# Kernel tuning notes

Hardware: AMD Instinct MI355X
Metric: run time of the kernel (lower is better)

## Reference

```python
import jax, jax.numpy as jnp
import numpy as np

TEMPERATURE = 0.1
LARGE_NUM = 1e9


def _l2_normalize(x, eps=1e-12):
    # tf.math.l2_normalize: x * rsqrt(max(sum(x^2), eps))
    sq = jnp.sum(x * x, axis=-1, keepdims=True)
    return x * jax.lax.rsqrt(jnp.maximum(sq, eps))


def setup_inputs() -> dict:
    key = jax.random.key(0)
    k1, k2 = jax.random.split(key)
    B, D = 4096, 128
    z1 = jax.random.normal(k1, (B, D), dtype=jnp.float32)
    z2 = jax.random.normal(k2, (B, D), dtype=jnp.float32)
    return {"z1": z1, "z2": z2}


def reference(z1, z2):
    B = z1.shape[0]
    a = _l2_normalize(z1)  # [B, D]
    b = _l2_normalize(z2)  # [B, D]
    mask = jnp.eye(B, dtype=a.dtype)
    inv_t = 1.0 / TEMPERATURE
    logits_aa = jnp.matmul(a, a.T) * inv_t - mask * LARGE_NUM  # [B, B]
    logits_bb = jnp.matmul(b, b.T) * inv_t - mask * LARGE_NUM  # [B, B]
    logits_ab = jnp.matmul(a, b.T) * inv_t                      # [B, B]
    logits_ba = jnp.matmul(b, a.T) * inv_t                      # [B, B]
    part1 = jax.nn.softmax(jnp.concatenate([logits_ab, logits_aa], axis=1), axis=-1)
    part2 = jax.nn.softmax(jnp.concatenate([logits_ba, logits_bb], axis=1), axis=-1)
    return jnp.concatenate([part1, part2], axis=1)  # [B, 4B]
```

## Files before the change

### kernel.cpp

```cpp
#include <hip/hip_runtime.h>
#include <hip/hip_fp16.h>
#include <cstdint>
#include <cstddef>

#define NB   4096
#define ND   128
#define OUTW 16384

#define K2   14.4269504088896341f

typedef _Float16 f16;
typedef __attribute__((ext_vector_type(2))) _Float16 f16x2;
typedef __attribute__((ext_vector_type(8))) _Float16 f16x8;
typedef __attribute__((ext_vector_type(4))) float   f32x4;

__global__ __launch_bounds__(256) void nrm_kernel(const float* __restrict__ z1,
                                                  const float* __restrict__ z2,
                                                  f16* __restrict__ ab,
                                                  float* __restrict__ rowsum) {
  if (threadIdx.x < 4) rowsum[blockIdx.x * 4 + threadIdx.x] = 0.0f;
  int row  = blockIdx.x * 4 + (threadIdx.x >> 6);
  int lane = threadIdx.x & 63;
  const float* src = (row < NB) ? (z1 + (size_t)row * ND)
                                : (z2 + (size_t)(row - NB) * ND);
  float2 v = ((const float2*)src)[lane];
  float ss = v.x * v.x + v.y * v.y;
#pragma unroll
  for (int off = 32; off; off >>= 1) ss += __shfl_xor(ss, off);
  float r = rsqrtf(fmaxf(ss, 1e-12f));
  f16x2 h;
  h.x = (f16)(v.x * r);
  h.y = (f16)(v.y * r);
  ((f16x2*)(ab + (size_t)row * ND))[lane] = h;
}

template <bool WRITE>
__global__ __launch_bounds__(256) void pass_kernel(const f16* __restrict__ ab,
                                                   float* __restrict__ rowsum,
                                                   float* __restrict__ out) {
  __shared__ f16 As[128 * ND];
  __shared__ f16 Bs[128 * ND];
  __shared__ float cs[128];

  const int t    = threadIdx.x;
  const int wave = t >> 6;
  const int lane = t & 63;
  const int rt   = blockIdx.y;
  const int ct   = blockIdx.x;
  const int type = rt >> 5;
  const int r0   = (rt & 31) * 128;
  const int c0l  = ct * 128;
  const int h2   = (c0l >= NB) ? 1 : 0;
  const int c0   = c0l & (NB - 1);
  const bool diag = h2 && (c0 == r0);
  const f16* Q = ab + (size_t)type * NB * ND;
  const f16* K = ab + (size_t)(h2 ^ type ^ 1) * NB * ND;

  {
    int sub = t >> 4;
    int oct = t & 15;
#pragma unroll
    for (int i = 0; i < 8; ++i) {
      int rowl = i * 16 + sub;
      int goct = oct ^ (rowl & 15);
      const f16* ga = Q + (size_t)(r0 + rowl) * ND + goct * 8;
      const f16* gb = K + (size_t)(c0 + rowl) * ND + goct * 8;
      __builtin_amdgcn_global_load_lds(
          (const __attribute__((address_space(1))) void*)ga,
          (__attribute__((address_space(3))) void*)(As + rowl * ND + oct * 8),
          16, 0, 0);
      __builtin_amdgcn_global_load_lds(
          (const __attribute__((address_space(1))) void*)gb,
          (__attribute__((address_space(3))) void*)(Bs + rowl * ND + oct * 8),
          16, 0, 0);
    }
  }
  if (WRITE) {
    if (t < 128) {
      float s = rowsum[rt * 128 + t];
      cs[t] = -__log2f(s) - K2;
    }
  }
  __syncthreads();

  const int wr   = wave >> 1;
  const int wc   = wave & 1;
  const int quad = lane >> 4;
  const int l16  = lane & 15;

  f32x4 acc[4][4] = {};
#pragma unroll
  for (int ks = 0; ks < 4; ++ks) {
    f16x8 af[4], bf[4];
    int oct = ks * 4 + quad;
    int sw  = (oct ^ l16) * 8;
#pragma unroll
    for (int mi = 0; mi < 4; ++mi)
      af[mi] = *(const f16x8*)(As + (wr * 64 + mi * 16 + l16) * ND + sw);
#pragma unroll
    for (int ni = 0; ni < 4; ++ni)
      bf[ni] = *(const f16x8*)(Bs + (wc * 64 + ni * 16 + l16) * ND + sw);
#pragma unroll
    for (int mi = 0; mi < 4; ++mi)
#pragma unroll
      for (int ni = 0; ni < 4; ++ni)
        acc[mi][ni] = __builtin_amdgcn_mfma_f32_16x16x32_f16(af[mi], bf[ni],
                                                             acc[mi][ni], 0, 0, 0);
  }

  if (WRITE) {
    float4 cf[4];
#pragma unroll
    for (int mi = 0; mi < 4; ++mi)
      cf[mi] = *(const float4*)&cs[wr * 64 + mi * 16 + quad * 4];
#pragma unroll
    for (int mi = 0; mi < 4; ++mi) {
#pragma unroll
      for (int ni = 0; ni < 4; ++ni) {
        int col_l = wc * 64 + ni * 16 + l16;
        int cg    = c0l + col_l;
        int rbase = wr * 64 + mi * 16 + quad * 4;
        const float* cp = &cf[mi].x;
#pragma unroll
        for (int r = 0; r < 4; ++r) {
          int row_l = rbase + r;
          int rg    = r0 + row_l;
          float e = __builtin_amdgcn_exp2f(fmaf(acc[mi][ni][r], K2, cp[r]));
          if (diag) { if (col_l == row_l) e = 0.0f; }
          out[(size_t)rg * OUTW + (size_t)type * 8192 + cg] = e;
        }
      }
    }
  } else {
#pragma unroll
    for (int mi = 0; mi < 4; ++mi) {
      float ps[4] = {0.f, 0.f, 0.f, 0.f};
#pragma unroll
      for (int ni = 0; ni < 4; ++ni) {
        int col_l = wc * 64 + ni * 16 + l16;
        int rbase = wr * 64 + mi * 16 + quad * 4;
#pragma unroll
        for (int r = 0; r < 4; ++r) {
          float e = __builtin_amdgcn_exp2f(fmaf(acc[mi][ni][r], K2, -K2));
          if (diag) { if (col_l == rbase + r) e = 0.0f; }
          ps[r] += e;
        }
      }
#pragma unroll
      for (int r = 0; r < 4; ++r) {
        float v = ps[r];
#pragma unroll
        for (int off = 1; off < 16; off <<= 1) v += __shfl_xor(v, off);
        if (l16 == 0) {
          int row_l = wr * 64 + mi * 16 + quad * 4 + r;
          atomicAdd(&rowsum[rt * 128 + row_l], v);
        }
      }
    }
  }
}

extern "C" void kernel_launch(void* const* d_in, const int* in_sizes, int n_in,
                              void* d_out, int out_size, void* d_ws, size_t ws_size,
                              hipStream_t stream) {
  const float* z1 = (const float*)d_in[0];
  const float* z2 = (const float*)d_in[1];
  float* out = (float*)d_out;

  f16* ab = (f16*)d_ws;
  float* rowsum = (float*)((char*)d_ws + (size_t)8192 * ND * sizeof(f16));

  nrm_kernel<<<2048, 256, 0, stream>>>(z1, z2, ab, rowsum);
  dim3 grid(64, 64);
  pass_kernel<false><<<grid, 256, 0, stream>>>(ab, rowsum, out);
  pass_kernel<true><<<grid, 256, 0, stream>>>(ab, rowsum, out);
}
```

Before: 356.7 us.

## Keep Q fragments in registers and stream double-buffered K tiles per block

Each block now owns a 128-row strip and loops over 8 column tiles of 64, instead of handling one 128x128 tile per block. The Q operand is loaded once into registers and reused across every column tile, while the K tiles are double-buffered in LDS through async global-to-LDS loads. Row partial sums are kept in registers across the whole strip, so each block issues far fewer atomics. The intent is to cut redundant Q loads, atomic traffic and block launch overhead, at the cost of fewer blocks (1024), higher register pressure and a serialized loop per block.

New measurement: 305.5 us. 14.4% less time.

```diff
diff --git a/kernel.cpp b/kernel.cpp
--- a/kernel.cpp
+++ b/kernel.cpp
@@ -6,6 +6,8 @@
 #define NB   4096
 #define ND   128
 #define OUTW 16384
+#define CG   16
+#define IT   (8192 / CG / 64)
 
 #define K2   14.4269504088896341f
 
@@ -35,120 +37,138 @@
 }
 
 template <bool WRITE>
-__global__ __launch_bounds__(256) void pass_kernel(const f16* __restrict__ ab,
-                                                   float* __restrict__ rowsum,
-                                                   float* __restrict__ out) {
-  __shared__ f16 As[128 * ND];
-  __shared__ f16 Bs[128 * ND];
+__global__ __launch_bounds__(256, 2) void pass_kernel(const f16* __restrict__ ab,
+                                                      float* __restrict__ rowsum,
+                                                      float* __restrict__ out) {
+  __shared__ f16 Bs[2][64 * ND];
   __shared__ float cs[128];
 
   const int t    = threadIdx.x;
   const int wave = t >> 6;
   const int lane = t & 63;
-  const int rt   = blockIdx.y;
-  const int ct   = blockIdx.x;
-  const int type = rt >> 5;
-  const int r0   = (rt & 31) * 128;
-  const int c0l  = ct * 128;
-  const int h2   = (c0l >= NB) ? 1 : 0;
-  const int c0   = c0l & (NB - 1);
-  const bool diag = h2 && (c0 == r0);
-  const f16* Q = ab + (size_t)type * NB * ND;
-  const f16* K = ab + (size_t)(h2 ^ type ^ 1) * NB * ND;
-
-  {
-    int sub = t >> 4;
-    int oct = t & 15;
-#pragma unroll
-    for (int i = 0; i < 8; ++i) {
-      int rowl = i * 16 + sub;
-      int goct = oct ^ (rowl & 15);
-      const f16* ga = Q + (size_t)(r0 + rowl) * ND + goct * 8;
-      const f16* gb = K + (size_t)(c0 + rowl) * ND + goct * 8;
-      __builtin_amdgcn_global_load_lds(
-          (const __attribute__((address_space(1))) void*)ga,
-          (__attribute__((address_space(3))) void*)(As + rowl * ND + oct * 8),
-          16, 0, 0);
-      __builtin_amdgcn_global_load_lds(
-          (const __attribute__((address_space(1))) void*)gb,
-          (__attribute__((address_space(3))) void*)(Bs + rowl * ND + oct * 8),
-          16, 0, 0);
-    }
-  }
-  if (WRITE) {
-    if (t < 128) {
-      float s = rowsum[rt * 128 + t];
-      cs[t] = -__log2f(s) - K2;
-    }
-  }
-  __syncthreads();
-
   const int wr   = wave >> 1;
   const int wc   = wave & 1;
   const int quad = lane >> 4;
   const int l16  = lane & 15;
 
-  f32x4 acc[4][4] = {};
-#pragma unroll
-  for (int ks = 0; ks < 4; ++ks) {
-    f16x8 af[4], bf[4];
-    int oct = ks * 4 + quad;
-    int sw  = (oct ^ l16) * 8;
-#pragma unroll
-    for (int mi = 0; mi < 4; ++mi)
-      af[mi] = *(const f16x8*)(As + (wr * 64 + mi * 16 + l16) * ND + sw);
-#pragma unroll
-    for (int ni = 0; ni < 4; ++ni)
-      bf[ni] = *(const f16x8*)(Bs + (wc * 64 + ni * 16 + l16) * ND + sw);
+  const int rt    = blockIdx.y;
+  const int type  = rt >> 5;
+  const int r0    = (rt & 31) * 128;
+  const int g     = blockIdx.x;
+  const int h2    = (g >= CG / 2) ? 1 : 0;
+  const int cbl   = g * (8192 / CG);
+  const int cbase = cbl & (NB - 1);
+  const f16* Q  = ab + (size_t)type * NB * ND;
+  const f16* Kp = ab + (size_t)(h2 ? type : (type ^ 1)) * NB * ND;
+
+  f16x8 af[4][4];
+  {
+    const int arow = r0 + wr * 64 + l16;
 #pragma unroll
     for (int mi = 0; mi < 4; ++mi)
 #pragma unroll
-      for (int ni = 0; ni < 4; ++ni)
-        acc[mi][ni] = __builtin_amdgcn_mfma_f32_16x16x32_f16(af[mi], bf[ni],
-                                                             acc[mi][ni], 0, 0, 0);
+      for (int ks = 0; ks < 4; ++ks)
+        af[mi][ks] = *(const f16x8*)(Q + (size_t)(arow + mi * 16) * ND +
+                                     ks * 32 + quad * 8);
   }
 
-  if (WRITE) {
-    float4 cf[4];
+  const int sub = t >> 4;
+  const int oct = t & 15;
+  auto stage_b = [&](f16* buf, int kc0) {
+#pragma unroll
+    for (int i = 0; i < 4; ++i) {
+      int rowl = i * 16 + sub;
+      int goct = oct ^ (rowl & 15);
+      __builtin_amdgcn_global_load_lds(
+          (const __attribute__((address_space(1))) void*)(
+              Kp + (size_t)(kc0 + rowl) * ND + goct * 8),
+          (__attribute__((address_space(3))) void*)(buf + rowl * ND + oct * 8),
+          16, 0, 0);
+    }
+  };
+
+  float ps[4][4];
+  if (!WRITE) {
 #pragma unroll
     for (int mi = 0; mi < 4; ++mi)
-      cf[mi] = *(const float4*)&cs[wr * 64 + mi * 16 + quad * 4];
 #pragma unroll
-    for (int mi = 0; mi < 4; ++mi) {
+      for (int r = 0; r < 4; ++r) ps[mi][r] = 0.0f;
+  }
+
+  stage_b(Bs[0], cbase);
+  if (WRITE) {
+    if (t < 128) cs[t] = -__log2f(rowsum[rt * 128 + t]) - K2;
+  }
+  __syncthreads();
+
+  for (int it = 0; it < IT; ++it) {
+    if (it + 1 < IT) stage_b(Bs[(it + 1) & 1], cbase + (it + 1) * 64);
+
+    const f16* buf = Bs[it & 1];
+    f32x4 acc[4][2] = {};
 #pragma unroll
-      for (int ni = 0; ni < 4; ++ni) {
-        int col_l = wc * 64 + ni * 16 + l16;
-        int cg    = c0l + col_l;
-        int rbase = wr * 64 + mi * 16 + quad * 4;
+    for (int ks = 0; ks < 4; ++ks) {
+      int sw = (((ks * 4 + quad) ^ l16)) * 8;
+      f16x8 bf0 = *(const f16x8*)(buf + (wc * 32 + l16) * ND + sw);
+      f16x8 bf1 = *(const f16x8*)(buf + (wc * 32 + 16 + l16) * ND + sw);
+#pragma unroll
+      for (int mi = 0; mi < 4; ++mi) {
+        acc[mi][0] = __builtin_amdgcn_mfma_f32_16x16x32_f16(af[mi][ks], bf0,
+                                                            acc[mi][0], 0, 0, 0);
+        acc[mi][1] = __builtin_amdgcn_mfma_f32_16x16x32_f16(af[mi][ks], bf1,
+                                                            acc[mi][1], 0, 0, 0);
+      }
+    }
+
+    const int c0m = cbase + it * 64;
+    const bool dtile = h2 && (c0m == r0 || c0m == r0 + 64);
+
+    if (WRITE) {
+      float4 cf[4];
+#pragma unroll
+      for (int mi = 0; mi < 4; ++mi)
+        cf[mi] = *(const float4*)&cs[wr * 64 + mi * 16 + quad * 4];
+#pragma unroll
+      for (int mi = 0; mi < 4; ++mi) {
         const float* cp = &cf[mi].x;
 #pragma unroll
-        for (int r = 0; r < 4; ++r) {
-          int row_l = rbase + r;
-          int rg    = r0 + row_l;
-          float e = __builtin_amdgcn_exp2f(fmaf(acc[mi][ni][r], K2, cp[r]));
-          if (diag) { if (col_l == row_l) e = 0.0f; }
-          out[(size_t)rg * OUTW + (size_t)type * 8192 + cg] = e;
+        for (int ni = 0; ni < 2; ++ni) {
+          int col_l = wc * 32 + ni * 16 + l16;
+          size_t cout = (size_t)type * 8192 + cbl + it * 64 + col_l;
+#pragma unroll
+          for (int r = 0; r < 4; ++r) {
+            int row_l = wr * 64 + mi * 16 + quad * 4 + r;
+            float e = __builtin_amdgcn_exp2f(fmaf(acc[mi][ni][r], K2, cp[r]));
+            if (dtile && (c0m + col_l == r0 + row_l)) e = 0.0f;
+            out[(size_t)(r0 + row_l) * OUTW + cout] = e;
+          }
+        }
+      }
+    } else {
+#pragma unroll
+      for (int mi = 0; mi < 4; ++mi) {
+#pragma unroll
+        for (int ni = 0; ni < 2; ++ni) {
+          int col_l = wc * 32 + ni * 16 + l16;
+#pragma unroll
+          for (int r = 0; r < 4; ++r) {
+            int row_l = wr * 64 + mi * 16 + quad * 4 + r;
+            float e = __builtin_amdgcn_exp2f(fmaf(acc[mi][ni][r], K2, -K2));
+            if (dtile && (c0m + col_l == r0 + row_l)) e = 0.0f;
+            ps[mi][r] += e;
+          }
         }
       }
     }
-  } else {
+    __syncthreads();
+  }
+
+  if (!WRITE) {
 #pragma unroll
-    for (int mi = 0; mi < 4; ++mi) {
-      float ps[4] = {0.f, 0.f, 0.f, 0.f};
-#pragma unroll
-      for (int ni = 0; ni < 4; ++ni) {
-        int col_l = wc * 64 + ni * 16 + l16;
-        int rbase = wr * 64 + mi * 16 + quad * 4;
-#pragma unroll
-        for (int r = 0; r < 4; ++r) {
-          float e = __builtin_amdgcn_exp2f(fmaf(acc[mi][ni][r], K2, -K2));
-          if (diag) { if (col_l == rbase + r) e = 0.0f; }
-          ps[r] += e;
-        }
-      }
+    for (int mi = 0; mi < 4; ++mi)
 #pragma unroll
       for (int r = 0; r < 4; ++r) {
-        float v = ps[r];
+        float v = ps[mi][r];
 #pragma unroll
         for (int off = 1; off < 16; off <<= 1) v += __shfl_xor(v, off);
         if (l16 == 0) {
@@ -156,7 +176,6 @@
           atomicAdd(&rowsum[rt * 128 + row_l], v);
         }
       }
-    }
   }
 }
 
@@ -171,7 +190,7 @@
   float* rowsum = (float*)((char*)d_ws + (size_t)8192 * ND * sizeof(f16));
 
   nrm_kernel<<<2048, 256, 0, stream>>>(z1, z2, ab, rowsum);
-  dim3 grid(64, 64);
+  dim3 grid(CG, 64);
   pass_kernel<false><<<grid, 256, 0, stream>>>(ab, rowsum, out);
   pass_kernel<true><<<grid, 256, 0, stream>>>(ab, rowsum, out);
 }
```
